# Kernel optimization log

Measured on AMD Instinct MI355X. Metric: run time of the kernel, lower is better.

## Reference

```python
import jax, jax.numpy as jnp
import numpy as np

EPS = 1e-12  # torch F.normalize eps


def setup_inputs() -> dict:
    key = jax.random.key(0)
    k1, k2, k3 = jax.random.split(key, 3)
    N, C, H, W, K = 32, 128, 112, 112, 64
    x = jax.random.normal(k1, (N, C, H, W), dtype=jnp.float32)
    conv_w = jax.random.normal(k2, (K, C), dtype=jnp.float32) * 0.05  # 1x1 conv weight, no bias (vladv2=False)
    centroids = jax.random.uniform(k3, (K, C), dtype=jnp.float32)
    return {"x": x, "conv_w": conv_w, "centroids": centroids}


def reference(x, conv_w, centroids):
    N, C = x.shape[:2]
    K = centroids.shape[0]
    xf = x.reshape(N, C, -1)                       # (N, C, S)
    # 1x1 conv == per-pixel linear: (K,C) @ (N,C,S) -> (N,K,S)
    soft_assign = jnp.einsum('kc,ncs->nks', conv_w, xf)
    soft_assign = jax.nn.softmax(soft_assign, axis=1)  # softmax over clusters
    # vlad[n,k,c] = sum_s a[n,k,s] * (x[n,c,s] - cent[k,c])
    vlad = jnp.einsum('nks,ncs->nkc', soft_assign, xf) \
         - soft_assign.sum(axis=-1)[..., None] * centroids[None, :, :]
    # intra-normalize over descriptor dim
    vlad = vlad / jnp.maximum(jnp.linalg.norm(vlad, axis=2, keepdims=True), EPS)
    vlad = vlad.reshape(N, K * C)
    vlad = vlad / jnp.maximum(jnp.linalg.norm(vlad, axis=1, keepdims=True), EPS)
    return vlad
```

## Files before the change

### kernel.cpp

```cpp
#include <hip/hip_runtime.h>
#include <hip/hip_bf16.h>

#define NV_N 32
#define NV_C 128
#define NV_K 64
#define NV_S 12544
#define ST 64
#define TILES 14
#define SCHUNK 14
#define XC 72
#define XS2 132
#define AS 72

typedef short short8 __attribute__((ext_vector_type(8)));
typedef short short4v __attribute__((ext_vector_type(4)));
typedef float floatx4 __attribute__((ext_vector_type(4)));

static __device__ __forceinline__ unsigned short f2bf(float f) {
  union { float f; unsigned u; } v; v.f = f;
  unsigned r = v.u + 0x7FFFu + ((v.u >> 16) & 1u);
  return (unsigned short)(r >> 16);
}
static __device__ __forceinline__ unsigned pk2(float a, float b) {
  union { __hip_bfloat162 h; unsigned u; } v;
  v.h = __float22bfloat162_rn(make_float2(a, b));
  return v.u;
}
static __device__ __forceinline__ short8 pack8(float4 a, float4 b) {
  union { unsigned u[4]; short8 s; } r;
  r.u[0] = pk2(a.x, a.y); r.u[1] = pk2(a.z, a.w);
  r.u[2] = pk2(b.x, b.y); r.u[3] = pk2(b.z, b.w);
  return r.s;
}

__global__ __launch_bounds__(256, 2) void netvlad_main(
    const float* __restrict__ x, const float* __restrict__ conv_w,
    float* __restrict__ vlad_ws, float* __restrict__ asum_ws) {
  __shared__ __attribute__((aligned(16))) unsigned short x_c[NV_C * XC];
  __shared__ __attribute__((aligned(16))) unsigned short x_s[ST * XS2];
  __shared__ __attribute__((aligned(16))) unsigned short a_lds[NV_K * AS];
  __shared__ float asum_sh[4][NV_K];

  const int t = threadIdx.x;
  const int n = blockIdx.x / SCHUNK;
  const int chunk = blockIdx.x % SCHUNK;
  const int s_base = chunk * (ST * TILES);
  const int w = t >> 6;
  const int lane = t & 63;
  const int q = lane >> 4;
  const int l = lane & 15;

  const float* __restrict__ xn = x + (size_t)n * NV_C * NV_S;

  short8 wfrag[4][4];
#pragma unroll
  for (int mt = 0; mt < 4; ++mt)
#pragma unroll
    for (int kc = 0; kc < 4; ++kc) {
      const float* wp = conv_w + (mt * 16 + l) * NV_C + kc * 32 + q * 8;
      wfrag[mt][kc] = pack8(*(const float4*)wp, *(const float4*)(wp + 4));
    }

  floatx4 acc2[4][2];
  float asum_acc[4][4];
#pragma unroll
  for (int mt = 0; mt < 4; ++mt) {
#pragma unroll
    for (int nt = 0; nt < 2; ++nt) acc2[mt][nt] = (floatx4){0.f, 0.f, 0.f, 0.f};
#pragma unroll
    for (int r = 0; r < 4; ++r) asum_acc[mt][r] = 0.f;
  }

  float4 pf[8];
#pragma unroll
  for (int g = 0; g < 4; ++g) {
    int vec2 = t + g * 256; int c = vec2 >> 3; int sv8 = vec2 & 7;
    const float* p = xn + (size_t)c * NV_S + s_base + sv8 * 8;
    pf[2 * g] = *(const float4*)p;
    pf[2 * g + 1] = *(const float4*)(p + 4);
  }

  for (int tt = 0; tt < TILES; ++tt) {
    __syncthreads();

#pragma unroll
    for (int g = 0; g < 4; ++g) {
      int vec2 = t + g * 256; int c = vec2 >> 3; int sv8 = vec2 & 7;
      union { short8 s; unsigned short us[8]; } pk;
      pk.s = pack8(pf[2 * g], pf[2 * g + 1]);
      *(short8*)&x_c[c * XC + sv8 * 8] = pk.s;
#pragma unroll
      for (int j = 0; j < 8; ++j)
        x_s[(sv8 * 8 + j) * XS2 + c] = pk.us[j];
    }
    __syncthreads();

    if (tt + 1 < TILES) {
      const int s0n = s_base + (tt + 1) * ST;
#pragma unroll
      for (int g = 0; g < 4; ++g) {
        int vec2 = t + g * 256; int c = vec2 >> 3; int sv8 = vec2 & 7;
        const float* p = xn + (size_t)c * NV_S + s0n + sv8 * 8;
        pf[2 * g] = *(const float4*)p;
        pf[2 * g + 1] = *(const float4*)(p + 4);
      }
    }

    floatx4 acc1[4];
#pragma unroll
    for (int mt = 0; mt < 4; ++mt) acc1[mt] = (floatx4){0.f, 0.f, 0.f, 0.f};
#pragma unroll
    for (int kc = 0; kc < 4; ++kc) {
      union { short4v h[2]; short8 s8; } bfr;
      const unsigned short* bp = &x_s[(w * 16 + l) * XS2 + kc * 32 + q * 8];
      bfr.h[0] = *(const short4v*)bp;
      bfr.h[1] = *(const short4v*)(bp + 4);
#pragma unroll
      for (int mt = 0; mt < 4; ++mt)
        acc1[mt] = __builtin_amdgcn_mfma_f32_16x16x32_bf16(wfrag[mt][kc], bfr.s8, acc1[mt], 0, 0, 0);
    }

    {
      float sum = 0.f;
#pragma unroll
      for (int mt = 0; mt < 4; ++mt)
#pragma unroll
        for (int r = 0; r < 4; ++r) {
          float e = __expf(acc1[mt][r]);
          acc1[mt][r] = e; sum += e;
        }
      sum += __shfl_xor(sum, 16);
      sum += __shfl_xor(sum, 32);
      const float inv = 1.0f / sum;
#pragma unroll
      for (int mt = 0; mt < 4; ++mt)
#pragma unroll
        for (int r = 0; r < 4; ++r) {
          float a = acc1[mt][r] * inv;
          asum_acc[mt][r] += a;
          a_lds[(mt * 16 + q * 4 + r) * AS + w * 16 + l] = f2bf(a);
        }
    }
    __syncthreads();

#pragma unroll
    for (int sk = 0; sk < 2; ++sk) {
      short8 afr[4];
#pragma unroll
      for (int mt = 0; mt < 4; ++mt)
        afr[mt] = *(const short8*)&a_lds[(mt * 16 + l) * AS + sk * 32 + q * 8];
#pragma unroll
      for (int nt = 0; nt < 2; ++nt) {
        const short8 bfr = *(const short8*)&x_c[((w * 2 + nt) * 16 + l) * XC + sk * 32 + q * 8];
#pragma unroll
        for (int mt = 0; mt < 4; ++mt)
          acc2[mt][nt] = __builtin_amdgcn_mfma_f32_16x16x32_bf16(afr[mt], bfr, acc2[mt][nt], 0, 0, 0);
      }
    }
  }

#pragma unroll
  for (int mt = 0; mt < 4; ++mt)
#pragma unroll
    for (int r = 0; r < 4; ++r) {
      float v = asum_acc[mt][r];
      v += __shfl_xor(v, 1); v += __shfl_xor(v, 2);
      v += __shfl_xor(v, 4); v += __shfl_xor(v, 8);
      if (l == 0) asum_sh[w][mt * 16 + q * 4 + r] = v;
    }
  __syncthreads();
  const size_t slab = (size_t)(n * SCHUNK + chunk);
  if (t < NV_K)
    asum_ws[slab * NV_K + t] =
        asum_sh[0][t] + asum_sh[1][t] + asum_sh[2][t] + asum_sh[3][t];

  float* vw = vlad_ws + slab * (NV_K * NV_C);
#pragma unroll
  for (int mt = 0; mt < 4; ++mt)
#pragma unroll
    for (int nt = 0; nt < 2; ++nt)
#pragma unroll
      for (int r = 0; r < 4; ++r)
        vw[(mt * 16 + q * 4 + r) * NV_C + (w * 2 + nt) * 16 + l] = acc2[mt][nt][r];
}

__global__ __launch_bounds__(256) void netvlad_reduce(
    const float* __restrict__ vlad_ws, const float* __restrict__ asum_ws,
    const float* __restrict__ cent, float* __restrict__ vlad_f) {
  const int t = threadIdx.x;
  const int n = blockIdx.x >> 3;
  const int k = (blockIdx.x & 7) * 8 + (t >> 5);
  const int c4 = (t & 31) * 4;

  float as = 0.f;
  float4 acc = {0.f, 0.f, 0.f, 0.f};
#pragma unroll
  for (int ch = 0; ch < SCHUNK; ++ch) {
    const size_t slab = (size_t)(n * SCHUNK + ch);
    as += asum_ws[slab * NV_K + k];
    float4 p = *(const float4*)&vlad_ws[slab * (NV_K * NV_C) + k * NV_C + c4];
    acc.x += p.x; acc.y += p.y; acc.z += p.z; acc.w += p.w;
  }
  float4 ce = *(const float4*)&cent[k * NV_C + c4];
  float4 v;
  v.x = acc.x - as * ce.x; v.y = acc.y - as * ce.y;
  v.z = acc.z - as * ce.z; v.w = acc.w - as * ce.w;
  *(float4*)&vlad_f[(size_t)n * (NV_K * NV_C) + k * NV_C + c4] = v;
}

__global__ __launch_bounds__(256) void netvlad_finalize(
    const float* __restrict__ vlad_f, float* __restrict__ out) {
  __shared__ float v_lds[NV_K * NV_C];
  __shared__ float red4[256];
  __shared__ float rscale[NV_K];
  __shared__ float gscale_sh;

  const int t = threadIdx.x; const int n = blockIdx.x;
  const float* vf = vlad_f + (size_t)n * (NV_K * NV_C);

#pragma unroll
  for (int i = 0; i < 8; ++i) {
    int vec = t + i * 256; int k = vec >> 5; int cq = vec & 31;
    *(float4*)&v_lds[k * NV_C + cq * 4] = *(const float4*)(vf + k * NV_C + cq * 4);
  }
  __syncthreads();

  {
    const int k = t >> 2, part = t & 3;
    const float* row = &v_lds[k * NV_C + part * 32];
    float ss = 0.0f;
#pragma unroll
    for (int c = 0; c < 32; ++c) { float v = row[c]; ss += v * v; }
    red4[t] = ss;
  }
  __syncthreads();
  if (t < NV_K) {
    float ss = red4[t * 4] + red4[t * 4 + 1] + red4[t * 4 + 2] + red4[t * 4 + 3];
    rscale[t] = 1.0f / fmaxf(sqrtf(ss), 1e-12f);
  }
  __syncthreads();

  float gp = 0.0f;
#pragma unroll
  for (int i = 0; i < 8; ++i) {
    int vec = t + i * 256; int k = vec >> 5; int cq = vec & 31;
    float4 v = *(const float4*)&v_lds[k * NV_C + cq * 4];
    float rs = rscale[k];
    gp += (v.x * v.x + v.y * v.y + v.z * v.z + v.w * v.w) * rs * rs;
  }
  red4[t] = gp;
  __syncthreads();
  if (t < 64) {
    float s = red4[t] + red4[t + 64] + red4[t + 128] + red4[t + 192];
#pragma unroll
    for (int o = 32; o > 0; o >>= 1) s += __shfl_down(s, o);
    if (t == 0) gscale_sh = 1.0f / fmaxf(sqrtf(s), 1e-12f);
  }
  __syncthreads();
  const float gs = gscale_sh;

#pragma unroll
  for (int i = 0; i < 8; ++i) {
    int vec = t + i * 256; int k = vec >> 5; int cq = vec & 31;
    float4 v = *(const float4*)&v_lds[k * NV_C + cq * 4];
    const float sc = rscale[k] * gs;
    v.x *= sc; v.y *= sc; v.z *= sc; v.w *= sc;
    *(float4*)(out + (size_t)n * (NV_K * NV_C) + k * NV_C + cq * 4) = v;
  }
}

extern "C" void kernel_launch(void* const* d_in, const int* in_sizes, int n_in,
                              void* d_out, int out_size, void* d_ws, size_t ws_size,
                              hipStream_t stream) {
  (void)in_sizes; (void)n_in; (void)out_size; (void)ws_size;
  const float* x      = (const float*)d_in[0];
  const float* conv_w = (const float*)d_in[1];
  const float* cent   = (const float*)d_in[2];
  float* out = (float*)d_out;

  float* vlad_ws = (float*)d_ws;
  float* asum_ws = vlad_ws + (size_t)NV_N * SCHUNK * NV_K * NV_C;
  float* vlad_f  = asum_ws + (size_t)NV_N * SCHUNK * NV_K;

  hipLaunchKernelGGL(netvlad_main, dim3(NV_N * SCHUNK), dim3(256), 0, stream,
                     x, conv_w, vlad_ws, asum_ws);
  hipLaunchKernelGGL(netvlad_reduce, dim3(NV_N * 8), dim3(256), 0, stream,
                     vlad_ws, asum_ws, cent, vlad_f);
  hipLaunchKernelGGL(netvlad_finalize, dim3(NV_N), dim3(256), 0, stream,
                     vlad_f, out);
}
```

Measured before the change: 301.8 us.

## Load x MFMA fragments directly from global, drop LDS staging of x

Removes the shared-memory x_c/x_s tiles and their transposed scatter stores. Each wave now loads its MFMA B-operand fragments for both GEMMs straight from global memory and packs them to bf16 in registers. The softmax-assignment LDS buffer is double-buffered, which drops two of the three barriers per tile. The cost is that x is read twice from global and the software prefetch is gone. The first GEMM's loads are strided scalar reads, 32 per thread per tile, so this leans on the caches and may add latency.

```diff
diff --git a/kernel.cpp b/kernel.cpp
--- a/kernel.cpp
+++ b/kernel.cpp
@@ -8,12 +8,9 @@
 #define ST 64
 #define TILES 14
 #define SCHUNK 14
-#define XC 72
-#define XS2 132
 #define AS 72
 
 typedef short short8 __attribute__((ext_vector_type(8)));
-typedef short short4v __attribute__((ext_vector_type(4)));
 typedef float floatx4 __attribute__((ext_vector_type(4)));
 
 static __device__ __forceinline__ unsigned short f2bf(float f) {
@@ -32,13 +29,17 @@
   r.u[2] = pk2(b.x, b.y); r.u[3] = pk2(b.z, b.w);
   return r.s;
 }
+static __device__ __forceinline__ short8 pack8s(const float* f) {
+  union { unsigned u[4]; short8 s; } r;
+  r.u[0] = pk2(f[0], f[1]); r.u[1] = pk2(f[2], f[3]);
+  r.u[2] = pk2(f[4], f[5]); r.u[3] = pk2(f[6], f[7]);
+  return r.s;
+}
 
 __global__ __launch_bounds__(256, 2) void netvlad_main(
     const float* __restrict__ x, const float* __restrict__ conv_w,
     float* __restrict__ vlad_ws, float* __restrict__ asum_ws) {
-  __shared__ __attribute__((aligned(16))) unsigned short x_c[NV_C * XC];
-  __shared__ __attribute__((aligned(16))) unsigned short x_s[ST * XS2];
-  __shared__ __attribute__((aligned(16))) unsigned short a_lds[NV_K * AS];
+  __shared__ __attribute__((aligned(16))) unsigned short a_lds[2][NV_K * AS];
   __shared__ float asum_sh[4][NV_K];
 
   const int t = threadIdx.x;
@@ -71,39 +72,28 @@
     for (int r = 0; r < 4; ++r) asum_acc[mt][r] = 0.f;
   }
 
-  float4 pf[8];
-#pragma unroll
-  for (int g = 0; g < 4; ++g) {
-    int vec2 = t + g * 256; int c = vec2 >> 3; int sv8 = vec2 & 7;
-    const float* p = xn + (size_t)c * NV_S + s_base + sv8 * 8;
-    pf[2 * g] = *(const float4*)p;
-    pf[2 * g + 1] = *(const float4*)(p + 4);
-  }
+  const float* __restrict__ xg1 = xn + (size_t)(q * 8) * NV_S + s_base + w * 16 + l;
+  const float* __restrict__ xg2a = xn + (size_t)((w * 2 + 0) * 16 + l) * NV_S + s_base + q * 8;
+  const float* __restrict__ xg2b = xn + (size_t)((w * 2 + 1) * 16 + l) * NV_S + s_base + q * 8;
 
   for (int tt = 0; tt < TILES; ++tt) {
-    __syncthreads();
-
-#pragma unroll
-    for (int g = 0; g < 4; ++g) {
-      int vec2 = t + g * 256; int c = vec2 >> 3; int sv8 = vec2 & 7;
-      union { short8 s; unsigned short us[8]; } pk;
-      pk.s = pack8(pf[2 * g], pf[2 * g + 1]);
-      *(short8*)&x_c[c * XC + sv8 * 8] = pk.s;
+    const int buf = tt & 1;
+    const int so = tt * ST;
+
+    float bxf[4][8];
+#pragma unroll
+    for (int kc = 0; kc < 4; ++kc)
 #pragma unroll
       for (int j = 0; j < 8; ++j)
-        x_s[(sv8 * 8 + j) * XS2 + c] = pk.us[j];
-    }
-    __syncthreads();
-
-    if (tt + 1 < TILES) {
-      const int s0n = s_base + (tt + 1) * ST;
-#pragma unroll
-      for (int g = 0; g < 4; ++g) {
-        int vec2 = t + g * 256; int c = vec2 >> 3; int sv8 = vec2 & 7;
-        const float* p = xn + (size_t)c * NV_S + s0n + sv8 * 8;
-        pf[2 * g] = *(const float4*)p;
-        pf[2 * g + 1] = *(const float4*)(p + 4);
-      }
+        bxf[kc][j] = xg1[(size_t)(kc * 32 + j) * NV_S + so];
+
+    float4 p2[2][2][2];
+#pragma unroll
+    for (int sk = 0; sk < 2; ++sk) {
+      p2[0][sk][0] = *(const float4*)(xg2a + so + sk * 32);
+      p2[0][sk][1] = *(const float4*)(xg2a + so + sk * 32 + 4);
+      p2[1][sk][0] = *(const float4*)(xg2b + so + sk * 32);
+      p2[1][sk][1] = *(const float4*)(xg2b + so + sk * 32 + 4);
     }
 
     floatx4 acc1[4];
@@ -111,13 +101,10 @@
     for (int mt = 0; mt < 4; ++mt) acc1[mt] = (floatx4){0.f, 0.f, 0.f, 0.f};
 #pragma unroll
     for (int kc = 0; kc < 4; ++kc) {
-      union { short4v h[2]; short8 s8; } bfr;
-      const unsigned short* bp = &x_s[(w * 16 + l) * XS2 + kc * 32 + q * 8];
-      bfr.h[0] = *(const short4v*)bp;
-      bfr.h[1] = *(const short4v*)(bp + 4);
-#pragma unroll
-      for (int mt = 0; mt < 4; ++mt)
-        acc1[mt] = __builtin_amdgcn_mfma_f32_16x16x32_bf16(wfrag[mt][kc], bfr.s8, acc1[mt], 0, 0, 0);
+      const short8 bfr = pack8s(bxf[kc]);
+#pragma unroll
+      for (int mt = 0; mt < 4; ++mt)
+        acc1[mt] = __builtin_amdgcn_mfma_f32_16x16x32_bf16(wfrag[mt][kc], bfr, acc1[mt], 0, 0, 0);
     }
 
     {
@@ -138,7 +125,7 @@
         for (int r = 0; r < 4; ++r) {
           float a = acc1[mt][r] * inv;
           asum_acc[mt][r] += a;
-          a_lds[(mt * 16 + q * 4 + r) * AS + w * 16 + l] = f2bf(a);
+          a_lds[buf][(mt * 16 + q * 4 + r) * AS + w * 16 + l] = f2bf(a);
         }
     }
     __syncthreads();
@@ -148,10 +135,10 @@
       short8 afr[4];
 #pragma unroll
       for (int mt = 0; mt < 4; ++mt)
-        afr[mt] = *(const short8*)&a_lds[(mt * 16 + l) * AS + sk * 32 + q * 8];
+        afr[mt] = *(const short8*)&a_lds[buf][(mt * 16 + l) * AS + sk * 32 + q * 8];
 #pragma unroll
       for (int nt = 0; nt < 2; ++nt) {
-        const short8 bfr = *(const short8*)&x_c[((w * 2 + nt) * 16 + l) * XC + sk * 32 + q * 8];
+        const short8 bfr = pack8(p2[nt][sk][0], p2[nt][sk][1]);
 #pragma unroll
         for (int mt = 0; mt < 4; ++mt)
           acc2[mt][nt] = __builtin_amdgcn_mfma_f32_16x16x32_bf16(afr[mt], bfr, acc2[mt][nt], 0, 0, 0);
```

After: 309.9 us. 1.03x slower.
